# Performance work log

Hardware: AMD Instinct MI355X
Metric: run time of the kernel (lower is better)

Reference implementation:

```python
import jax, jax.numpy as jnp
import numpy as np

K_MSG = 1024   # message length k (rows of G)
N_CODE = 2048  # codeword length n (cols of G)
B = 32768      # number of message blocks


def setup_inputs() -> dict:
    key = jax.random.key(0)
    kb, kg = jax.random.split(key)
    b = jax.random.randint(kb, (B, K_MSG), 0, 2, dtype=jnp.int32)
    G = jax.random.randint(kg, (K_MSG, N_CODE), 0, 2, dtype=jnp.int32)
    return {"b": b, "G": G}


def reference(b, G):
    # GF(2) linear block encode: c = (b @ G) mod 2
    # b: [num_blocks, k] bits (0/1), G: [k, n] generator matrix (0/1)
    b2 = b.astype(jnp.int32)
    G2 = G.astype(jnp.int32)
    c = jnp.mod(jnp.matmul(b2, G2), 2)  # [num_blocks, n]
    return c.astype(jnp.int32)
```

## Files before the change

kernel.cpp:

```cpp
#include <hip/hip_runtime.h>
#include <stdint.h>

typedef unsigned int u32;
typedef int v4i  __attribute__((ext_vector_type(4)));
typedef int v16i __attribute__((ext_vector_type(16)));

#define K_MSG   1024
#define N_CODE  2048
#define NB      32768

__global__ void pack_gBF(const int* __restrict__ G, u32* __restrict__ bf) {
    int idx = blockIdx.x * blockDim.x + threadIdx.x;
    const int j  = idx & (N_CODE - 1);
    const int kq = idx >> 11;
    u32 p = 0;
#pragma unroll
    for (int i = 0; i < 4; ++i) {
        int v = G[(size_t)(kq * 4 + i) * N_CODE + j];
        p |= (u32)(v & 1) << (8 * i);
    }
    const int jb = j >> 5, jr = j & 31;
    const int kb = kq >> 3, hi = (kq >> 2) & 1, b4 = kq & 3;
    bf[(size_t)(jb * 32 + kb) * 256 + hi * 128 + jr * 4 + b4] = p;
}


#define MFMA_I8(va, vb, vc) __builtin_amdgcn_mfma_i32_32x32x32_i8(va, vb, vc, 0, 0, 0)

#define MFMA_SET(sfx) do {                              \
    acc[0][0] = MFMA_I8(a0##sfx, b0##sfx, acc[0][0]);   \
    acc[0][1] = MFMA_I8(a0##sfx, b1##sfx, acc[0][1]);   \
    acc[0][2] = MFMA_I8(a0##sfx, b2##sfx, acc[0][2]);   \
    acc[0][3] = MFMA_I8(a0##sfx, b3##sfx, acc[0][3]);   \
    acc[1][0] = MFMA_I8(a1##sfx, b0##sfx, acc[1][0]);   \
    acc[1][1] = MFMA_I8(a1##sfx, b1##sfx, acc[1][1]);   \
    acc[1][2] = MFMA_I8(a1##sfx, b2##sfx, acc[1][2]);   \
    acc[1][3] = MFMA_I8(a1##sfx, b3##sfx, acc[1][3]);   \
} while (0)

#define LOAD_SET(sfx, s_) do {                                      \
    int ao_ = lr * 1024 + ((((s_) * 32) + hi * 16) ^ axor);         \
    a0##sfx = *(const v4i*)(As + ao_);                              \
    a1##sfx = *(const v4i*)(As + ao_ + 32768);                      \
    b0##sfx = *(const v4i*)(bp0 + (size_t)(s_) * 1024);             \
    b1##sfx = *(const v4i*)(bp1 + (size_t)(s_) * 1024);             \
    b2##sfx = *(const v4i*)(bp2 + (size_t)(s_) * 1024);             \
    b3##sfx = *(const v4i*)(bp3 + (size_t)(s_) * 1024);             \
} while (0)

__global__ __launch_bounds__(256, 2) void gemm_fused(const int* __restrict__ b,
                                                     const char* __restrict__ bf,
                                                     int* __restrict__ out) {
    __shared__ __align__(16) char As[64 * 1024];

    const int t  = threadIdx.x;
    const int m0 = blockIdx.x * 64;
    const int w = t >> 6, lane = t & 63, lr = lane & 31, hi = lane >> 5;
    const int axor = (lr & 7) << 4;

    {
        const int* src = b + (size_t)m0 * K_MSG;
#pragma unroll 8
        for (int i = 0; i < 64; ++i) {
            int4 v = *(const int4*)(src + (size_t)i * K_MSG + t * 4);
            u32 p = (u32)(v.x & 1) | ((u32)(v.y & 1) << 8) |
                    ((u32)(v.z & 1) << 16) | ((u32)(v.w & 1) << 24);
            *(u32*)(As + i * 1024 + ((t * 4) ^ ((i & 7) << 4))) = p;
        }
    }
    __syncthreads();

#pragma unroll 1
    for (int pass = 0; pass < 4; ++pass) {
        const char* bp0 = bf + ((size_t)pass * 16 + w * 4) * 32768 + lane * 16;
        const char* bp1 = bp0 + 32768;
        const char* bp2 = bp0 + 65536;
        const char* bp3 = bp0 + 98304;

        v16i acc[2][4] = {};
        v4i a0A, a1A, b0A, b1A, b2A, b3A;
        v4i a0B, a1B, b0B, b1B, b2B, b3B;
        v4i a0C, a1C, b0C, b1C, b2C, b3C;
        v4i a0D, a1D, b0D, b1D, b2D, b3D;

        LOAD_SET(A, 0);
        LOAD_SET(B, 1);
#pragma unroll 1
        for (int s = 0; s < 32; s += 4) {
            LOAD_SET(C, s + 2);
            LOAD_SET(D, s + 3);
            MFMA_SET(A);
            MFMA_SET(B);
            if (s + 4 < 32) {
                LOAD_SET(A, s + 4);
                LOAD_SET(B, s + 5);
            }
            MFMA_SET(C);
            MFMA_SET(D);
        }

#pragma unroll
        for (int mi = 0; mi < 2; ++mi) {
#pragma unroll
            for (int ni = 0; ni < 4; ++ni) {
                const int cbase = pass * 512 + w * 128 + ni * 32 + lr;
                const int rbase = m0 + mi * 32 + 4 * hi;
#pragma unroll
                for (int r = 0; r < 16; ++r) {
                    const int row = rbase + (r & 3) + 8 * (r >> 2);
                    out[(size_t)row * N_CODE + cbase] = acc[mi][ni][r] & 1;
                }
            }
        }
    }
}

__global__ void encode_naive(const int* __restrict__ b, const int* __restrict__ G,
                             int* __restrict__ out) {
    size_t idx = (size_t)blockIdx.x * blockDim.x + threadIdx.x;
    size_t total = (size_t)NB * N_CODE;
    if (idx >= total) return;
    int i = (int)(idx / N_CODE);
    int j = (int)(idx % N_CODE);
    int acc = 0;
    for (int k = 0; k < K_MSG; ++k)
        acc ^= b[(size_t)i * K_MSG + k] & G[(size_t)k * N_CODE + j];
    out[idx] = acc & 1;
}

extern "C" void kernel_launch(void* const* d_in, const int* in_sizes, int n_in,
                              void* d_out, int out_size, void* d_ws, size_t ws_size,
                              hipStream_t stream) {
    const int* b = (const int*)d_in[0];
    const int* G = (const int*)d_in[1];
    int* out = (int*)d_out;

    const size_t bf_bytes = (size_t)N_CODE * K_MSG;

    if (ws_size < bf_bytes) {
        size_t total = (size_t)NB * N_CODE;
        encode_naive<<<(unsigned)((total + 255) / 256), 256, 0, stream>>>(b, G, out);
        return;
    }

    char* bf = (char*)d_ws;

    pack_gBF<<<2048, 256, 0, stream>>>(G, (u32*)bf);
    gemm_fused<<<NB / 64, 256, 0, stream>>>(b, bf, out);
}
```

Baseline: 166.5 us.

## Split N across blocks and emit bit-packed output expanded by a separate kernel

The GEMM grid now gives each block a single 512-column slice instead of looping four passes, with a swizzled block-to-tile mapping so the four blocks sharing a row tile run close together. Results are bit-packed into a small workspace buffer with wave ballots. A new expand_bits kernel then writes the full int32 output with contiguous vector stores. This targets the scattered, per-element output stores and the long serial per-block pass loop. In exchange, each message tile is loaded and packed four times (once per column slice), and there is an extra kernel launch plus an intermediate buffer round trip.

After: 222.3 us. +33.5%, slower.

```diff
diff --git a/kernel.cpp b/kernel.cpp
--- a/kernel.cpp
+++ b/kernel.cpp
@@ -2,6 +2,7 @@
 #include <stdint.h>
 
 typedef unsigned int u32;
+typedef unsigned long long u64;
 typedef int v4i  __attribute__((ext_vector_type(4)));
 typedef int v16i __attribute__((ext_vector_type(16)));
 
@@ -48,13 +49,17 @@
     b3##sfx = *(const v4i*)(bp3 + (size_t)(s_) * 1024);             \
 } while (0)
 
-__global__ __launch_bounds__(256, 2) void gemm_fused(const int* __restrict__ b,
-                                                     const char* __restrict__ bf,
-                                                     int* __restrict__ out) {
+__global__ __launch_bounds__(256, 2) void gemm_i8(const int* __restrict__ b,
+                                                  const char* __restrict__ bf,
+                                                  u32* __restrict__ pk) {
     __shared__ __align__(16) char As[64 * 1024];
 
-    const int t  = threadIdx.x;
-    const int m0 = blockIdx.x * 64;
+    const int t   = threadIdx.x;
+    const int bid = blockIdx.x;
+    const int swz = (bid & 7) * 256 + (bid >> 3);
+    const int m0  = (swz >> 2) * 64;
+    const int n0  = (swz & 3) * 512;
+
     const int w = t >> 6, lane = t & 63, lr = lane & 31, hi = lane >> 5;
     const int axor = (lr & 7) << 4;
 
@@ -70,48 +75,63 @@
     }
     __syncthreads();
 
+    const char* bp0 = bf + ((size_t)(n0 >> 5) + w * 4) * 32768 + lane * 16;
+    const char* bp1 = bp0 + 32768;
+    const char* bp2 = bp0 + 65536;
+    const char* bp3 = bp0 + 98304;
+
+    v16i acc[2][4] = {};
+    v4i a0A, a1A, b0A, b1A, b2A, b3A;
+    v4i a0B, a1B, b0B, b1B, b2B, b3B;
+    v4i a0C, a1C, b0C, b1C, b2C, b3C;
+    v4i a0D, a1D, b0D, b1D, b2D, b3D;
+
+    LOAD_SET(A, 0);
+    LOAD_SET(B, 1);
 #pragma unroll 1
-    for (int pass = 0; pass < 4; ++pass) {
-        const char* bp0 = bf + ((size_t)pass * 16 + w * 4) * 32768 + lane * 16;
-        const char* bp1 = bp0 + 32768;
-        const char* bp2 = bp0 + 65536;
-        const char* bp3 = bp0 + 98304;
-
-        v16i acc[2][4] = {};
-        v4i a0A, a1A, b0A, b1A, b2A, b3A;
-        v4i a0B, a1B, b0B, b1B, b2B, b3B;
-        v4i a0C, a1C, b0C, b1C, b2C, b3C;
-        v4i a0D, a1D, b0D, b1D, b2D, b3D;
-
-        LOAD_SET(A, 0);
-        LOAD_SET(B, 1);
-#pragma unroll 1
-        for (int s = 0; s < 32; s += 4) {
-            LOAD_SET(C, s + 2);
-            LOAD_SET(D, s + 3);
-            MFMA_SET(A);
-            MFMA_SET(B);
-            if (s + 4 < 32) {
-                LOAD_SET(A, s + 4);
-                LOAD_SET(B, s + 5);
-            }
-            MFMA_SET(C);
-            MFMA_SET(D);
+    for (int s = 0; s < 32; s += 4) {
+        LOAD_SET(C, s + 2);
+        LOAD_SET(D, s + 3);
+        MFMA_SET(A);
+        MFMA_SET(B);
+        if (s + 4 < 32) {
+            LOAD_SET(A, s + 4);
+            LOAD_SET(B, s + 5);
         }
+        MFMA_SET(C);
+        MFMA_SET(D);
+    }
 
 #pragma unroll
-        for (int mi = 0; mi < 2; ++mi) {
+    for (int mi = 0; mi < 2; ++mi) {
 #pragma unroll
-            for (int ni = 0; ni < 4; ++ni) {
-                const int cbase = pass * 512 + w * 128 + ni * 32 + lr;
-                const int rbase = m0 + mi * 32 + 4 * hi;
+        for (int ni = 0; ni < 4; ++ni) {
+            const int cb = (n0 >> 5) + w * 4 + ni;
 #pragma unroll
-                for (int r = 0; r < 16; ++r) {
-                    const int row = rbase + (r & 3) + 8 * (r >> 2);
-                    out[(size_t)row * N_CODE + cbase] = acc[mi][ni][r] & 1;
+            for (int r = 0; r < 16; ++r) {
+                u64 m = __ballot((acc[mi][ni][r] & 1) != 0);
+                if (lane == r) {
+                    const int row0 = m0 + mi * 32 + (r & 3) + 8 * (r >> 2);
+                    pk[(size_t)row0 * 64 + cb]       = (u32)m;
+                    pk[(size_t)(row0 + 4) * 64 + cb] = (u32)(m >> 32);
                 }
             }
         }
+    }
+}
+
+__global__ void expand_bits(const u32* __restrict__ pk, int* __restrict__ out) {
+    const int idx = blockIdx.x * blockDim.x + threadIdx.x;
+    const u32 p = pk[idx];
+    int4* dst = (int4*)(out + (size_t)idx * 32);
+#pragma unroll
+    for (int q = 0; q < 8; ++q) {
+        int4 v;
+        v.x = (int)((p >> (4 * q))     & 1u);
+        v.y = (int)((p >> (4 * q + 1)) & 1u);
+        v.z = (int)((p >> (4 * q + 2)) & 1u);
+        v.w = (int)((p >> (4 * q + 3)) & 1u);
+        dst[q] = v;
     }
 }
 
@@ -136,15 +156,18 @@
     int* out = (int*)d_out;
 
     const size_t bf_bytes = (size_t)N_CODE * K_MSG;
+    const size_t pk_bytes = (size_t)NB * (N_CODE / 8);
 
-    if (ws_size < bf_bytes) {
+    if (ws_size < bf_bytes + pk_bytes) {
         size_t total = (size_t)NB * N_CODE;
         encode_naive<<<(unsigned)((total + 255) / 256), 256, 0, stream>>>(b, G, out);
         return;
     }
 
     char* bf = (char*)d_ws;
+    u32*  pk = (u32*)((char*)d_ws + bf_bytes);
 
     pack_gBF<<<2048, 256, 0, stream>>>(G, (u32*)bf);
-    gemm_fused<<<NB / 64, 256, 0, stream>>>(b, bf, out);
+    gemm_i8<<<2048, 256, 0, stream>>>(b, bf, pk);
+    expand_bits<<<(NB * N_CODE / 32) / 256, 256, 0, stream>>>(pk, out);
 }
```

## Stage output bits via ballot in LDS for coalesced vector stores; swizzle block order

Applied to the files above, without the earlier changes.

Instead of scattering 4-byte scalar stores per accumulator element, each wave ballots the parity bits into packed 32-bit words in double-buffered shared memory. After a barrier, the block writes full rows with 16-byte vector stores. Block indices are also remapped so consecutive blocks take strided row tiles. This targets the uncoalesced output write of a 256 MB result, at the cost of extra ballots, LDS traffic and a barrier per pass.

Result: faster. 138.9 us (-16.6%).

```diff
diff --git a/kernel.cpp b/kernel.cpp
--- a/kernel.cpp
+++ b/kernel.cpp
@@ -2,6 +2,7 @@
 #include <stdint.h>
 
 typedef unsigned int u32;
+typedef unsigned long long u64;
 typedef int v4i  __attribute__((ext_vector_type(4)));
 typedef int v16i __attribute__((ext_vector_type(16)));
 
@@ -48,13 +49,16 @@
     b3##sfx = *(const v4i*)(bp3 + (size_t)(s_) * 1024);             \
 } while (0)
 
-__global__ __launch_bounds__(256, 2) void gemm_fused(const int* __restrict__ b,
-                                                     const char* __restrict__ bf,
-                                                     int* __restrict__ out) {
+__global__ __launch_bounds__(256, 2) void gemm_all(const int* __restrict__ b,
+                                                   const char* __restrict__ bf,
+                                                   int* __restrict__ out) {
     __shared__ __align__(16) char As[64 * 1024];
+    __shared__ u32 pk[2][64 * 16];
 
-    const int t  = threadIdx.x;
-    const int m0 = blockIdx.x * 64;
+    const int t   = threadIdx.x;
+    const int bid = blockIdx.x;
+    const int m0  = ((bid & 7) * 64 + (bid >> 3)) * 64;
+
     const int w = t >> 6, lane = t & 63, lr = lane & 31, hi = lane >> 5;
     const int axor = (lr & 7) << 4;
 
@@ -72,6 +76,7 @@
 
 #pragma unroll 1
     for (int pass = 0; pass < 4; ++pass) {
+        const int cur = pass & 1;
         const char* bp0 = bf + ((size_t)pass * 16 + w * 4) * 32768 + lane * 16;
         const char* bp1 = bp0 + 32768;
         const char* bp2 = bp0 + 65536;
@@ -103,14 +108,38 @@
         for (int mi = 0; mi < 2; ++mi) {
 #pragma unroll
             for (int ni = 0; ni < 4; ++ni) {
-                const int cbase = pass * 512 + w * 128 + ni * 32 + lr;
-                const int rbase = m0 + mi * 32 + 4 * hi;
+                const int cbL = w * 4 + ni;
 #pragma unroll
                 for (int r = 0; r < 16; ++r) {
-                    const int row = rbase + (r & 3) + 8 * (r >> 2);
-                    out[(size_t)row * N_CODE + cbase] = acc[mi][ni][r] & 1;
+                    u64 m = __ballot((acc[mi][ni][r] & 1) != 0);
+                    if ((lane & 31) == r) {
+                        const int row = mi * 32 + (r & 3) + 8 * (r >> 2) + 4 * hi;
+                        pk[cur][row * 16 + cbL] = (u32)(m >> (hi * 32));
+                    }
                 }
             }
+        }
+        __syncthreads();
+
+        int* op = out + (size_t)m0 * N_CODE + pass * 512;
+#pragma unroll 1
+        for (int rr = 0; rr < 16; ++rr) {
+            const int row = w * 16 + rr;
+            const int sb  = (lane & 7) * 4;
+            u32 p0 = pk[cur][row * 16 + (lane >> 3)];
+            u32 p1 = pk[cur][row * 16 + 8 + (lane >> 3)];
+            v4i v0, v1;
+            v0.x = (int)((p0 >> (sb + 0)) & 1u);
+            v0.y = (int)((p0 >> (sb + 1)) & 1u);
+            v0.z = (int)((p0 >> (sb + 2)) & 1u);
+            v0.w = (int)((p0 >> (sb + 3)) & 1u);
+            v1.x = (int)((p1 >> (sb + 0)) & 1u);
+            v1.y = (int)((p1 >> (sb + 1)) & 1u);
+            v1.z = (int)((p1 >> (sb + 2)) & 1u);
+            v1.w = (int)((p1 >> (sb + 3)) & 1u);
+            int* dst = op + (size_t)row * N_CODE + lane * 4;
+            *(v4i*)dst         = v0;
+            *(v4i*)(dst + 256) = v1;
         }
     }
 }
@@ -146,5 +175,5 @@
     char* bf = (char*)d_ws;
 
     pack_gBF<<<2048, 256, 0, stream>>>(G, (u32*)bf);
-    gemm_fused<<<NB / 64, 256, 0, stream>>>(b, bf, out);
+    gemm_all<<<NB / 64, 256, 0, stream>>>(b, bf, out);
 }
```

## Warp-specialize GEMM: compute waves pack bits to LDS, store waves write output

Applied to the files above, without the earlier changes.

The block grows to 512 threads. Four waves run the int8 MFMA GEMM over eight narrower column passes with a 2x2 accumulator tile and pack the parity bits via ballot into a double-buffered LDS bit array. The other four waves expand those bits and write coalesced 16-byte output rows, overlapping the 256 MB output store with the next pass's compute. Block indices are also remapped to spread row tiles across XCDs. This adds a __syncthreads per pass and a smaller per-wave tile, so each compute wave reuses the loaded G fragments less.

New measurement: 154.7 us. 1.08x faster.

```diff
diff --git a/kernel.cpp b/kernel.cpp
--- a/kernel.cpp
+++ b/kernel.cpp
@@ -2,6 +2,7 @@
 #include <stdint.h>
 
 typedef unsigned int u32;
+typedef unsigned long long u64;
 typedef int v4i  __attribute__((ext_vector_type(4)));
 typedef int v16i __attribute__((ext_vector_type(16)));
 
@@ -27,89 +28,121 @@
 
 #define MFMA_I8(va, vb, vc) __builtin_amdgcn_mfma_i32_32x32x32_i8(va, vb, vc, 0, 0, 0)
 
-#define MFMA_SET(sfx) do {                              \
+#define MFMAS(sfx) do {                                 \
     acc[0][0] = MFMA_I8(a0##sfx, b0##sfx, acc[0][0]);   \
     acc[0][1] = MFMA_I8(a0##sfx, b1##sfx, acc[0][1]);   \
-    acc[0][2] = MFMA_I8(a0##sfx, b2##sfx, acc[0][2]);   \
-    acc[0][3] = MFMA_I8(a0##sfx, b3##sfx, acc[0][3]);   \
     acc[1][0] = MFMA_I8(a1##sfx, b0##sfx, acc[1][0]);   \
     acc[1][1] = MFMA_I8(a1##sfx, b1##sfx, acc[1][1]);   \
-    acc[1][2] = MFMA_I8(a1##sfx, b2##sfx, acc[1][2]);   \
-    acc[1][3] = MFMA_I8(a1##sfx, b3##sfx, acc[1][3]);   \
 } while (0)
 
-#define LOAD_SET(sfx, s_) do {                                      \
+#define LOADS(sfx, s_) do {                                         \
     int ao_ = lr * 1024 + ((((s_) * 32) + hi * 16) ^ axor);         \
     a0##sfx = *(const v4i*)(As + ao_);                              \
     a1##sfx = *(const v4i*)(As + ao_ + 32768);                      \
     b0##sfx = *(const v4i*)(bp0 + (size_t)(s_) * 1024);             \
     b1##sfx = *(const v4i*)(bp1 + (size_t)(s_) * 1024);             \
-    b2##sfx = *(const v4i*)(bp2 + (size_t)(s_) * 1024);             \
-    b3##sfx = *(const v4i*)(bp3 + (size_t)(s_) * 1024);             \
 } while (0)
 
-__global__ __launch_bounds__(256, 2) void gemm_fused(const int* __restrict__ b,
-                                                     const char* __restrict__ bf,
-                                                     int* __restrict__ out) {
+__global__ __launch_bounds__(512, 4) void gemm_ws(const int* __restrict__ b,
+                                                  const char* __restrict__ bf,
+                                                  int* __restrict__ out) {
     __shared__ __align__(16) char As[64 * 1024];
+    __shared__ u32 pk[2][64 * 8];
 
-    const int t  = threadIdx.x;
-    const int m0 = blockIdx.x * 64;
+    const int t   = threadIdx.x;
+    const int bid = blockIdx.x;
+    const int m0  = ((bid & 7) * 64 + (bid >> 3)) * 64;
+
     const int w = t >> 6, lane = t & 63, lr = lane & 31, hi = lane >> 5;
     const int axor = (lr & 7) << 4;
 
     {
         const int* src = b + (size_t)m0 * K_MSG;
 #pragma unroll 8
-        for (int i = 0; i < 64; ++i) {
-            int4 v = *(const int4*)(src + (size_t)i * K_MSG + t * 4);
+        for (int i2 = 0; i2 < 32; ++i2) {
+            const int i  = i2 * 2 + (t >> 8);
+            const int c4 = (t & 255) * 4;
+            int4 v = *(const int4*)(src + (size_t)i * K_MSG + c4);
             u32 p = (u32)(v.x & 1) | ((u32)(v.y & 1) << 8) |
                     ((u32)(v.z & 1) << 16) | ((u32)(v.w & 1) << 24);
-            *(u32*)(As + i * 1024 + ((t * 4) ^ ((i & 7) << 4))) = p;
+            *(u32*)(As + i * 1024 + (c4 ^ ((i & 7) << 4))) = p;
         }
     }
     __syncthreads();
 
+    if (w < 4) {
 #pragma unroll 1
-    for (int pass = 0; pass < 4; ++pass) {
-        const char* bp0 = bf + ((size_t)pass * 16 + w * 4) * 32768 + lane * 16;
-        const char* bp1 = bp0 + 32768;
-        const char* bp2 = bp0 + 65536;
-        const char* bp3 = bp0 + 98304;
+        for (int pass = 0; pass < 8; ++pass) {
+            const char* bp0 = bf + ((size_t)pass * 8 + w * 2) * 32768 + lane * 16;
+            const char* bp1 = bp0 + 32768;
 
-        v16i acc[2][4] = {};
-        v4i a0A, a1A, b0A, b1A, b2A, b3A;
-        v4i a0B, a1B, b0B, b1B, b2B, b3B;
-        v4i a0C, a1C, b0C, b1C, b2C, b3C;
-        v4i a0D, a1D, b0D, b1D, b2D, b3D;
+            v16i acc[2][2] = {};
+            v4i a0A, a1A, b0A, b1A;
+            v4i a0B, a1B, b0B, b1B;
 
-        LOAD_SET(A, 0);
-        LOAD_SET(B, 1);
+            LOADS(A, 0);
 #pragma unroll 1
-        for (int s = 0; s < 32; s += 4) {
-            LOAD_SET(C, s + 2);
-            LOAD_SET(D, s + 3);
-            MFMA_SET(A);
-            MFMA_SET(B);
-            if (s + 4 < 32) {
-                LOAD_SET(A, s + 4);
-                LOAD_SET(B, s + 5);
+            for (int s = 0; s < 32; s += 2) {
+                LOADS(B, s + 1);
+                MFMAS(A);
+                if (s + 2 < 32) LOADS(A, s + 2);
+                MFMAS(B);
             }
-            MFMA_SET(C);
-            MFMA_SET(D);
+
+            u32* pkc = pk[pass & 1];
+#pragma unroll
+            for (int mi = 0; mi < 2; ++mi) {
+#pragma unroll
+                for (int ni = 0; ni < 2; ++ni) {
+                    const int cbL = w * 2 + ni;
+#pragma unroll
+                    for (int r = 0; r < 16; ++r) {
+                        u64 m = __ballot((acc[mi][ni][r] & 1) != 0);
+                        if ((lane & 31) == r) {
+                            const int row = mi * 32 + (r & 3) + 8 * (r >> 2) + 4 * hi;
+                            pkc[row * 8 + cbL] = (u32)(m >> (hi * 32));
+                        }
+                    }
+                }
+            }
+            __syncthreads();
         }
-
+    } else {
+        const int sw = w - 4;
+#pragma unroll 1
+        for (int pass = 0; pass < 8; ++pass) {
+            if (pass > 0) {
+                const u32* pkp = pk[(pass - 1) & 1];
+                int* op = out + (size_t)m0 * N_CODE + (pass - 1) * 256;
 #pragma unroll
-        for (int mi = 0; mi < 2; ++mi) {
+                for (int rr = 0; rr < 16; ++rr) {
+                    const int row = sw * 16 + rr;
+                    const u32 pword = pkp[row * 8 + (lane >> 3)];
+                    const int sb = (lane & 7) * 4;
+                    v4i v;
+                    v.x = (int)((pword >> (sb + 0)) & 1u);
+                    v.y = (int)((pword >> (sb + 1)) & 1u);
+                    v.z = (int)((pword >> (sb + 2)) & 1u);
+                    v.w = (int)((pword >> (sb + 3)) & 1u);
+                    *(v4i*)(op + (size_t)row * N_CODE + lane * 4) = v;
+                }
+            }
+            __syncthreads();
+        }
+        {
+            const u32* pkp = pk[1];
+            int* op = out + (size_t)m0 * N_CODE + 7 * 256;
 #pragma unroll
-            for (int ni = 0; ni < 4; ++ni) {
-                const int cbase = pass * 512 + w * 128 + ni * 32 + lr;
-                const int rbase = m0 + mi * 32 + 4 * hi;
-#pragma unroll
-                for (int r = 0; r < 16; ++r) {
-                    const int row = rbase + (r & 3) + 8 * (r >> 2);
-                    out[(size_t)row * N_CODE + cbase] = acc[mi][ni][r] & 1;
-                }
+            for (int rr = 0; rr < 16; ++rr) {
+                const int row = sw * 16 + rr;
+                const u32 pword = pkp[row * 8 + (lane >> 3)];
+                const int sb = (lane & 7) * 4;
+                v4i v;
+                v.x = (int)((pword >> (sb + 0)) & 1u);
+                v.y = (int)((pword >> (sb + 1)) & 1u);
+                v.z = (int)((pword >> (sb + 2)) & 1u);
+                v.w = (int)((pword >> (sb + 3)) & 1u);
+                *(v4i*)(op + (size_t)row * N_CODE + lane * 4) = v;
             }
         }
     }
@@ -146,5 +179,5 @@
     char* bf = (char*)d_ws;
 
     pack_gBF<<<2048, 256, 0, stream>>>(G, (u32*)bf);
-    gemm_fused<<<NB / 64, 256, 0, stream>>>(b, bf, out);
+    gemm_ws<<<NB / 64, 512, 0, stream>>>(b, bf, out);
 }
```
